# Kernel tuning notes

Hardware: AMD Instinct MI355X
Metric: run time of the kernel (lower is better)

## Reference

```python
import jax, jax.numpy as jnp
import numpy as np

N, H, MSG, OUT = 512, 128, 128, 64
F1, F2 = 256, 256  # f_dims (also used for g_mlp per source)
GOUT = 128         # hardcoded output_gmlp_dim
O1 = 256           # o_dims


def _p(key, shape, scale):
    return jax.random.normal(key, shape, dtype=jnp.float32) * scale


def setup_inputs() -> dict:
    key = jax.random.key(0)
    ks = jax.random.split(key, 24)
    s = lambda fan_in: 1.0 / np.sqrt(fan_in)
    inp = {
        "x": jax.random.normal(ks[0], (N, H), dtype=jnp.float32),
        "hidden": jax.random.normal(ks[1], (N, H), dtype=jnp.float32),
        "h0": jnp.zeros((1, N, H), dtype=jnp.float32),
        "c0": jnp.zeros((1, N, H), dtype=jnp.float32),
        # f MLP: 2H -> F1 -> F2 -> MSG
        "Wf1": _p(ks[2], (F1, 2 * H), s(2 * H)), "bf1": jnp.zeros((F1,), jnp.float32),
        "Wf2": _p(ks[3], (F2, F1), s(F1)), "bf2": jnp.zeros((F2,), jnp.float32),
        "Wf3": _p(ks[4], (MSG, F2), s(F2)), "bf3": jnp.zeros((MSG,), jnp.float32),
        # g_mlp: H+MSG -> F1 -> F2 -> GOUT
        "Wg1": _p(ks[5], (F1, H + MSG), s(H + MSG)), "bg1": jnp.zeros((F1,), jnp.float32),
        "Wg2": _p(ks[6], (F2, F1), s(F1)), "bg2": jnp.zeros((F2,), jnp.float32),
        "Wg3": _p(ks[7], (GOUT, F2), s(F2)), "bg3": jnp.zeros((GOUT,), jnp.float32),
        # LSTM (1 layer): GOUT -> H, gate order i,f,g,o
        "W_ih": _p(ks[8], (4 * H, GOUT), s(H)), "W_hh": _p(ks[9], (4 * H, H), s(H)),
        "b_ih": jnp.zeros((4 * H,), jnp.float32), "b_hh": jnp.zeros((4 * H,), jnp.float32),
        # o MLP: H -> O1 -> OUT
        "Wo1": _p(ks[10], (O1, H), s(H)), "bo1": jnp.zeros((O1,), jnp.float32),
        "Wo2": _p(ks[11], (OUT, O1), s(O1)), "bo2": jnp.zeros((OUT,), jnp.float32),
    }
    return inp


def reference(x, hidden, h0, c0,
              Wf1, bf1, Wf2, bf2, Wf3, bf3,
              Wg1, bg1, Wg2, bg2, Wg3, bg3,
              W_ih, W_hh, b_ih, b_hh,
              Wo1, bo1, Wo2, bo2):
    # --- pairwise message MLP f(cat(hidden[i], hidden[j])) over all (i,j) ---
    # split first-layer weight to avoid materializing [N,N,2H] concat
    A = hidden @ Wf1[:, :H].T            # [N, F1], contribution of node i
    B = hidden @ Wf1[:, H:].T            # [N, F1], contribution of node j
    h1 = jax.nn.relu(A[:, None, :] + B[None, :, :] + bf1)   # [N, N, F1]
    h2 = jax.nn.relu(h1 @ Wf2.T + bf2)                       # [N, N, F2]
    messages = h2 @ Wf3.T + bf3                              # [N, N, MSG]
    sum_messages = jnp.sum(messages, axis=0)                 # [N, MSG] (sum over i)

    # --- g_mlp on cat(x, sum_messages) ---
    g_in = jnp.concatenate([x, sum_messages], axis=1)        # [N, H+MSG]
    g1 = jax.nn.relu(g_in @ Wg1.T + bg1)
    g2 = jax.nn.relu(g1 @ Wg2.T + bg2)
    input_g = g2 @ Wg3.T + bg3                               # [N, GOUT]

    # --- single-step LSTM (seq_len=1, batch=N), PyTorch gate order i,f,g,o ---
    gates = input_g @ W_ih.T + b_ih + h0[0] @ W_hh.T + b_hh  # [N, 4H]
    i_g, f_g, g_g, o_g = jnp.split(gates, 4, axis=1)
    i_g = jax.nn.sigmoid(i_g); f_g = jax.nn.sigmoid(f_g)
    g_g = jnp.tanh(g_g); o_g = jax.nn.sigmoid(o_g)
    c_new = f_g * c0[0] + i_g * g_g
    hidden_new = o_g * jnp.tanh(c_new)                       # [N, H]

    # --- output MLP o (single_output=False) ---
    o1 = jax.nn.relu(hidden_new @ Wo1.T + bo1)
    out = o1 @ Wo2.T + bo2                                   # [N, OUT]

    return (out, hidden_new, hidden_new[None], c_new[None])
```

## Files before the change

kernel.cpp:

```cpp
#include <hip/hip_runtime.h>
#include <hip/hip_bf16.h>


#define NN   512
#define HH   128
#define F1D  256
#define F2D  256
#define OUTD 64
#define ICHUNK 64

typedef _Float16 half_t;
typedef _Float16 half4 __attribute__((ext_vector_type(4)));
typedef _Float16 half8 __attribute__((ext_vector_type(8)));
typedef float float4_t __attribute__((ext_vector_type(4)));
typedef float float8_t __attribute__((ext_vector_type(8)));

__device__ __forceinline__ float sigmoidf_(float x) {
    return 1.0f / (1.0f + __expf(-x));
}

#define HL_INV 2.44140625e-4f

#define WS_TAIL_B 1835008
#define T3H 0
#define G1H 65536
#define G2H 196608
#define G3H 327680
#define CATH 393216
#define O1H 655360
#define O2H 720896

__constant__ int c_cumblk[7] = {32, 96, 160, 192, 320, 352, 368};
__constant__ int c_hioff[7]  = {T3H, G1H, G2H, G3H, CATH, O1H, O2H};
__constant__ int c_cnt[7]    = {32768, 65536, 65536, 32768, 131072, 32768, 16384};
__constant__ int c_K[7]      = {256, 256, 256, 256, 256, 128, 256};

__global__ __launch_bounds__(256)
void k0_prep(const float* __restrict__ Wf3,
             const float* __restrict__ Wg1, const float* __restrict__ Wg2,
             const float* __restrict__ Wg3,
             const float* __restrict__ W_ih, const float* __restrict__ W_hh,
             const float* __restrict__ Wo1, const float* __restrict__ Wo2,
             half_t* __restrict__ tail) {
    const int t = threadIdx.x;
    const int bid = blockIdx.x;
    int m = 0;
    while (m < 6 && bid >= c_cumblk[m]) ++m;
    const int startblk = (m == 0) ? 0 : c_cumblk[m - 1];
    const int e0 = (bid - startblk) * 1024 + t * 4;
    const int K = c_K[m];

    float4_t v;
    if (m == 4) {
        const int n = e0 >> 8, k = e0 & 255;
        v = (k < 128) ? *(const float4_t*)(W_ih + n * 128 + k)
                      : *(const float4_t*)(W_hh + n * 128 + (k - 128));
    } else {
        const float* src;
        switch (m) {
            case 0: src = Wf3; break;
            case 1: src = Wg1; break;
            case 2: src = Wg2; break;
            case 3: src = Wg3; break;
            case 5: src = Wo1; break;
            default: src = Wo2; break;
        }
        v = *(const float4_t*)(src + e0);
    }
    const int n = e0 / K, k = e0 % K;
    const int panel = n >> 4, l15 = n & 15;
    const int ks = k >> 5, g4 = (k >> 3) & 3, e = k & 7;
    const int fidx = panel * (K << 4) + ks * 512 + ((g4 << 4) + l15) * 8 + e;

    half4 hv, lv;
#pragma unroll
    for (int q = 0; q < 4; ++q) {
        half_t h = (half_t)v[q];
        hv[q] = h;
        lv[q] = (half_t)((v[q] - (float)h) * 4096.0f);
    }
    *(half4*)(tail + c_hioff[m] + fidx) = hv;
    *(half4*)(tail + c_hioff[m] + c_cnt[m] + fidx) = lv;
}

__global__ void k1_proj(const float* __restrict__ hidden,
                        const float* __restrict__ Wf1,
                        const float* __restrict__ bf1,
                        const float* __restrict__ Wf2,
                        float* __restrict__ A32,
                        float* __restrict__ B32,
                        half_t* __restrict__ Whi,
                        half_t* __restrict__ Wlo) {
    __shared__ float hid[4][HH];
    const int t = threadIdx.x;
    const int i0 = blockIdx.x * 4;
    for (int q = t; q < 4 * HH; q += 256)
        hid[q >> 7][q & 127] = hidden[(i0 + (q >> 7)) * HH + (q & 127)];
    __syncthreads();

    float accA[4], accB[4];
    const float b = bf1[t];
#pragma unroll
    for (int r = 0; r < 4; ++r) { accA[r] = b; accB[r] = 0.0f; }

    const float* wr = Wf1 + t * 256;
#pragma unroll 4
    for (int k = 0; k < HH; k += 4) {
        float4_t wa = *(const float4_t*)(wr + k);
        float4_t wb = *(const float4_t*)(wr + HH + k);
#pragma unroll
        for (int r = 0; r < 4; ++r) {
            const float* hp = &hid[r][k];
            accA[r] += wa[0]*hp[0] + wa[1]*hp[1] + wa[2]*hp[2] + wa[3]*hp[3];
            accB[r] += wb[0]*hp[0] + wb[1]*hp[1] + wb[2]*hp[2] + wb[3]*hp[3];
        }
    }
#pragma unroll
    for (int r = 0; r < 4; ++r) {
        A32[(i0 + r) * F1D + t] = accA[r];
        B32[(i0 + r) * F1D + t] = accB[r];
    }
    for (int q = t; q < 512; q += 256) {
        int idx = blockIdx.x * 512 + q;
        float wv = Wf2[idx];
        half_t hi = (half_t)wv;
        Whi[idx] = hi;
        Wlo[idx] = (half_t)((wv - (float)hi) * 4096.0f);
    }
}

__global__ __launch_bounds__(512, 2)
void k2_pairwise(const float* __restrict__ A32,
                 const float* __restrict__ B32,
                 const half_t* __restrict__ Whi,
                 const half_t* __restrict__ Wlo,
                 const float* __restrict__ bf2,
                 float* __restrict__ S) {
    __shared__ half_t hbuf[2][8][512];

    const int tid = threadIdx.x;
    const int lane = tid & 63;
    const int w = tid >> 6;
    const int l15 = lane & 15;
    const int g4 = lane >> 4;
    const int j0 = blockIdx.y * 16;
    const int i0 = blockIdx.x * ICHUNK;

    half8 Wh[2][8], Wl[2][8];
#pragma unroll
    for (int nt = 0; nt < 2; ++nt)
#pragma unroll
        for (int ks = 0; ks < 8; ++ks) {
            const size_t off = (size_t)(w*32 + nt*16 + l15) * F1D + ks*32 + g4*8;
            Wh[nt][ks] = *(const half8*)(Whi + off);
            Wl[nt][ks] = *(const half8*)(Wlo + off);
        }

    const float8_t Bw = *(const float8_t*)(B32 + (size_t)(j0 + l15) * F1D + w*32 + g4*8);

    float b2v[2];
#pragma unroll
    for (int nt = 0; nt < 2; ++nt) b2v[nt] = bf2[w*32 + nt*16 + l15];

    float4_t acc[2];
#pragma unroll
    for (int nt = 0; nt < 2; ++nt)
#pragma unroll
        for (int r = 0; r < 4; ++r) acc[nt][r] = 0.0f;

    {
        float8_t a = *(const float8_t*)(A32 + (size_t)i0 * F1D + w*32 + g4*8);
        float8_t s = a + Bw;
        half8 hf;
#pragma unroll
        for (int e = 0; e < 8; ++e) hf[e] = (half_t)fmaxf(s[e], 0.0f);
        *(half8*)&hbuf[0][w][lane * 8] = hf;
    }
    __syncthreads();

    int p = 0;
    for (int io = 0; io < ICHUNK; ++io) {
        float8_t a;
        if (io + 1 < ICHUNK)
            a = *(const float8_t*)(A32 + (size_t)(i0 + io + 1) * F1D + w*32 + g4*8);

        float4_t C[2], Cl[2];
#pragma unroll
        for (int nt = 0; nt < 2; ++nt)
#pragma unroll
            for (int r = 0; r < 4; ++r) { C[nt][r] = 0.0f; Cl[nt][r] = 0.0f; }

#pragma unroll
        for (int ks = 0; ks < 8; ++ks) {
            half8 hf = *(const half8*)&hbuf[p][ks][lane * 8];
            C[0]  = __builtin_amdgcn_mfma_f32_16x16x32_f16(hf, Wh[0][ks], C[0], 0, 0, 0);
            C[1]  = __builtin_amdgcn_mfma_f32_16x16x32_f16(hf, Wh[1][ks], C[1], 0, 0, 0);
            Cl[0] = __builtin_amdgcn_mfma_f32_16x16x32_f16(hf, Wl[0][ks], Cl[0], 0, 0, 0);
            Cl[1] = __builtin_amdgcn_mfma_f32_16x16x32_f16(hf, Wl[1][ks], Cl[1], 0, 0, 0);
        }

        if (io + 1 < ICHUNK) {
            float8_t s = a + Bw;
            half8 hf;
#pragma unroll
            for (int e = 0; e < 8; ++e) hf[e] = (half_t)fmaxf(s[e], 0.0f);
            *(half8*)&hbuf[p ^ 1][w][lane * 8] = hf;
        }

#pragma unroll
        for (int nt = 0; nt < 2; ++nt) {
#pragma unroll
            for (int r = 0; r < 4; ++r) {
                float v = fmaf(Cl[nt][r], HL_INV, C[nt][r]) + b2v[nt];
                acc[nt][r] += fmaxf(v, 0.0f);
            }
        }
        __syncthreads();
        p ^= 1;
    }

#pragma unroll
    for (int nt = 0; nt < 2; ++nt)
#pragma unroll
        for (int r = 0; r < 4; ++r)
            atomicAdd(&S[(size_t)(j0 + g4*4 + r) * F2D + w*32 + nt*16 + l15], acc[nt][r]);
}

#define AST 260

template<int NT, int NKS>
__device__ __forceinline__ void frag_gemm(const float* __restrict__ aPtr,
                                          const half_t* __restrict__ WhF,
                                          const half_t* __restrict__ WlF,
                                          const int* pB, int lane8,
                                          float4_t* Chi, float4_t* Clo) {
#pragma unroll
    for (int ks = 0; ks < NKS; ++ks) {
        float4_t a0 = *(const float4_t*)(aPtr + ks * 32);
        float4_t a1 = *(const float4_t*)(aPtr + ks * 32 + 4);
        half8 ah, al;
#pragma unroll
        for (int e = 0; e < 4; ++e) {
            half_t h0 = (half_t)a0[e];
            ah[e] = h0; al[e] = (half_t)((a0[e] - (float)h0) * 4096.0f);
            half_t h1 = (half_t)a1[e];
            ah[4+e] = h1; al[4+e] = (half_t)((a1[e] - (float)h1) * 4096.0f);
        }
#pragma unroll
        for (int nt = 0; nt < NT; ++nt) {
            half8 wh = *(const half8*)(WhF + pB[nt] + ks * 512 + lane8);
            half8 wl = *(const half8*)(WlF + pB[nt] + ks * 512 + lane8);
            Chi[nt] = __builtin_amdgcn_mfma_f32_16x16x32_f16(ah, wh, Chi[nt], 0, 0, 0);
            Clo[nt] = __builtin_amdgcn_mfma_f32_16x16x32_f16(ah, wl, Clo[nt], 0, 0, 0);
            Clo[nt] = __builtin_amdgcn_mfma_f32_16x16x32_f16(al, wh, Clo[nt], 0, 0, 0);
        }
    }
}

__global__ __launch_bounds__(512)
void k4_tail(const float* __restrict__ S,
             const float* __restrict__ x,
             const float* __restrict__ h0,
             const float* __restrict__ c0,
             const half_t* __restrict__ tail,
             const float* __restrict__ bf3,
             const float* __restrict__ bg1, const float* __restrict__ bg2,
             const float* __restrict__ bg3,
             const float* __restrict__ b_ih, const float* __restrict__ b_hh,
             const float* __restrict__ bo1, const float* __restrict__ bo2,
             float* __restrict__ out,
             float* __restrict__ hid_out,
             float* __restrict__ h_out,
             float* __restrict__ c_out) {
    __shared__ float bufA[16 * AST];
    __shared__ float bufB[16 * AST];
    __shared__ float bufC[16 * AST];
    const int tid = threadIdx.x;
    const int lane = tid & 63;
    const int w = tid >> 6;
    const int l15 = lane & 15;
    const int g4 = lane >> 4;
    const int r0 = blockIdx.x * 16;
    const int lane8 = lane * 8;

    for (int q = tid; q < 16 * 256; q += 512)
        bufC[(q >> 8) * AST + (q & 255)] = S[(size_t)(r0 + (q >> 8)) * 256 + (q & 255)];
    for (int q = tid; q < 16 * 128; q += 512)
        bufA[(q >> 7) * AST + (q & 127)] = x[(r0 + (q >> 7)) * 128 + (q & 127)];
    __syncthreads();

    const float* aFrag;
    int pB[4];
    float4_t Chi[4], Clo[4];

    {
        const int n = w * 16 + l15;
        pB[0] = w * 4096;
        Chi[0] = float4_t{0,0,0,0}; Clo[0] = float4_t{0,0,0,0};
        aFrag = bufC + l15 * AST + g4 * 8;
        frag_gemm<1, 8>(aFrag, tail + T3H, tail + T3H + 32768, pB, lane8, Chi, Clo);
        const float b = 512.0f * bf3[n];
#pragma unroll
        for (int r = 0; r < 4; ++r)
            bufA[(g4 * 4 + r) * AST + 128 + n] = Chi[0][r] + Clo[0][r] * HL_INV + b;
    }
    __syncthreads();

    {
        pB[0] = (w * 2) * 4096; pB[1] = (w * 2 + 1) * 4096;
        Chi[0] = float4_t{0,0,0,0}; Clo[0] = float4_t{0,0,0,0};
        Chi[1] = float4_t{0,0,0,0}; Clo[1] = float4_t{0,0,0,0};
        aFrag = bufA + l15 * AST + g4 * 8;
        frag_gemm<2, 8>(aFrag, tail + G1H, tail + G1H + 65536, pB, lane8, Chi, Clo);
#pragma unroll
        for (int nt = 0; nt < 2; ++nt) {
            const int n = w * 32 + nt * 16 + l15;
            const float b = bg1[n];
#pragma unroll
            for (int r = 0; r < 4; ++r)
                bufB[(g4 * 4 + r) * AST + n] = fmaxf(Chi[nt][r] + Clo[nt][r] * HL_INV + b, 0.0f);
        }
    }
    __syncthreads();

    {
        pB[0] = (w * 2) * 4096; pB[1] = (w * 2 + 1) * 4096;
        Chi[0] = float4_t{0,0,0,0}; Clo[0] = float4_t{0,0,0,0};
        Chi[1] = float4_t{0,0,0,0}; Clo[1] = float4_t{0,0,0,0};
        aFrag = bufB + l15 * AST + g4 * 8;
        frag_gemm<2, 8>(aFrag, tail + G2H, tail + G2H + 65536, pB, lane8, Chi, Clo);
#pragma unroll
        for (int nt = 0; nt < 2; ++nt) {
            const int n = w * 32 + nt * 16 + l15;
            const float b = bg2[n];
#pragma unroll
            for (int r = 0; r < 4; ++r)
                bufC[(g4 * 4 + r) * AST + n] = fmaxf(Chi[nt][r] + Clo[nt][r] * HL_INV + b, 0.0f);
        }
        for (int q = tid; q < 16 * 128; q += 512)
            bufA[(q >> 7) * AST + 128 + (q & 127)] = h0[(r0 + (q >> 7)) * 128 + (q & 127)];
    }
    __syncthreads();

    {
        const int n = w * 16 + l15;
        pB[0] = w * 4096;
        Chi[0] = float4_t{0,0,0,0}; Clo[0] = float4_t{0,0,0,0};
        aFrag = bufC + l15 * AST + g4 * 8;
        frag_gemm<1, 8>(aFrag, tail + G3H, tail + G3H + 32768, pB, lane8, Chi, Clo);
        const float b = bg3[n];
#pragma unroll
        for (int r = 0; r < 4; ++r)
            bufA[(g4 * 4 + r) * AST + n] = Chi[0][r] + Clo[0][r] * HL_INV + b;
    }
    __syncthreads();

    {
#pragma unroll
        for (int nt = 0; nt < 4; ++nt) {
            pB[nt] = (w + nt * 8) * 4096;
            Chi[nt] = float4_t{0,0,0,0}; Clo[nt] = float4_t{0,0,0,0};
        }
        aFrag = bufA + l15 * AST + g4 * 8;
        frag_gemm<4, 8>(aFrag, tail + CATH, tail + CATH + 131072, pB, lane8, Chi, Clo);

        const int nh = w * 16 + l15;
        float bi = b_ih[nh]       + b_hh[nh];
        float bf = b_ih[128 + nh] + b_hh[128 + nh];
        float bg = b_ih[256 + nh] + b_hh[256 + nh];
        float bo = b_ih[384 + nh] + b_hh[384 + nh];
#pragma unroll
        for (int r = 0; r < 4; ++r) {
            const int row = r0 + g4 * 4 + r;
            float gi = sigmoidf_(Chi[0][r] + Clo[0][r] * HL_INV + bi);
            float gf = sigmoidf_(Chi[1][r] + Clo[1][r] * HL_INV + bf);
            float gg = tanhf(    Chi[2][r] + Clo[2][r] * HL_INV + bg);
            float go = sigmoidf_(Chi[3][r] + Clo[3][r] * HL_INV + bo);
            float c = gf * c0[row * 128 + nh] + gi * gg;
            float h = go * tanhf(c);
            bufC[(g4 * 4 + r) * AST + nh] = h;
            hid_out[row * 128 + nh] = h;
            h_out[row * 128 + nh]   = h;
            c_out[row * 128 + nh]   = c;
        }
    }
    __syncthreads();

    {
        pB[0] = (w * 2) * 2048; pB[1] = (w * 2 + 1) * 2048;
        Chi[0] = float4_t{0,0,0,0}; Clo[0] = float4_t{0,0,0,0};
        Chi[1] = float4_t{0,0,0,0}; Clo[1] = float4_t{0,0,0,0};
        aFrag = bufC + l15 * AST + g4 * 8;
        frag_gemm<2, 4>(aFrag, tail + O1H, tail + O1H + 32768, pB, lane8, Chi, Clo);
#pragma unroll
        for (int nt = 0; nt < 2; ++nt) {
            const int n = w * 32 + nt * 16 + l15;
            const float b = bo1[n];
#pragma unroll
            for (int r = 0; r < 4; ++r)
                bufB[(g4 * 4 + r) * AST + n] = fmaxf(Chi[nt][r] + Clo[nt][r] * HL_INV + b, 0.0f);
        }
    }
    __syncthreads();

    if (w < 4) {
        const int n = w * 16 + l15;
        pB[0] = w * 4096;
        Chi[0] = float4_t{0,0,0,0}; Clo[0] = float4_t{0,0,0,0};
        aFrag = bufB + l15 * AST + g4 * 8;
        frag_gemm<1, 8>(aFrag, tail + O2H, tail + O2H + 16384, pB, lane8, Chi, Clo);
        const float b = bo2[n];
#pragma unroll
        for (int r = 0; r < 4; ++r)
            out[(r0 + g4 * 4 + r) * OUTD + n] = Chi[0][r] + Clo[0][r] * HL_INV + b;
    }
}

extern "C" void kernel_launch(void* const* d_in, const int* in_sizes, int n_in,
                              void* d_out, int out_size, void* d_ws, size_t ws_size,
                              hipStream_t stream) {
    const float* x      = (const float*)d_in[0];
    const float* hidden = (const float*)d_in[1];
    const float* h0     = (const float*)d_in[2];
    const float* c0     = (const float*)d_in[3];
    const float* Wf1    = (const float*)d_in[4];
    const float* bf1    = (const float*)d_in[5];
    const float* Wf2    = (const float*)d_in[6];
    const float* bf2    = (const float*)d_in[7];
    const float* Wf3    = (const float*)d_in[8];
    const float* bf3    = (const float*)d_in[9];
    const float* Wg1    = (const float*)d_in[10];
    const float* bg1    = (const float*)d_in[11];
    const float* Wg2    = (const float*)d_in[12];
    const float* bg2    = (const float*)d_in[13];
    const float* Wg3    = (const float*)d_in[14];
    const float* bg3    = (const float*)d_in[15];
    const float* W_ih   = (const float*)d_in[16];
    const float* W_hh   = (const float*)d_in[17];
    const float* b_ih   = (const float*)d_in[18];
    const float* b_hh   = (const float*)d_in[19];
    const float* Wo1    = (const float*)d_in[20];
    const float* bo1    = (const float*)d_in[21];
    const float* Wo2    = (const float*)d_in[22];
    const float* bo2    = (const float*)d_in[23];

    char* wsb = (char*)d_ws;
    float*  A32  = (float*)(wsb + 0);
    float*  B32  = (float*)(wsb + 524288);
    half_t* Whi  = (half_t*)(wsb + 1048576);
    half_t* Wlo  = (half_t*)(wsb + 1179648);
    float*  S    = (float*)(wsb + 1310720);
    half_t* tail = (half_t*)(wsb + WS_TAIL_B);

    float* outp  = (float*)d_out;
    float* hid1  = (float*)d_out + 32768;
    float* hid2  = (float*)d_out + 98304;
    float* cout  = (float*)d_out + 163840;

    hipMemsetAsync(S, 0, (size_t)NN * F2D * sizeof(float), stream);

    k0_prep<<<dim3(368), dim3(256), 0, stream>>>(Wf3, Wg1, Wg2, Wg3,
                                                 W_ih, W_hh, Wo1, Wo2, tail);

    k1_proj<<<dim3(128), dim3(256), 0, stream>>>(hidden, Wf1, bf1, Wf2,
                                                 A32, B32, Whi, Wlo);

    k2_pairwise<<<dim3(8, 32), dim3(512), 0, stream>>>(A32, B32, Whi, Wlo, bf2, S);

    k4_tail<<<dim3(32), dim3(512), 0, stream>>>(S, x, h0, c0, tail,
                                                bf3, bg1, bg2, bg3,
                                                b_ih, b_hh, bo1, bo2,
                                                outp, hid1, hid2, cout);
}
```

Measured before the change: 223.8 us.

## Pre-swizzle Wf2 into MFMA fragment layout and transpose Wf1 for coalesced projection

```diff
diff --git a/kernel.cpp b/kernel.cpp
--- a/kernel.cpp
+++ b/kernel.cpp
@@ -10,7 +10,6 @@
 #define ICHUNK 64
 
 typedef _Float16 half_t;
-typedef _Float16 half4 __attribute__((ext_vector_type(4)));
 typedef _Float16 half8 __attribute__((ext_vector_type(8)));
 typedef float float4_t __attribute__((ext_vector_type(4)));
 typedef float float8_t __attribute__((ext_vector_type(8)));
@@ -22,6 +21,7 @@
 #define HL_INV 2.44140625e-4f
 
 #define WS_TAIL_B 1835008
+#define WS_WT1_B  3342336
 #define T3H 0
 #define G1H 65536
 #define G2H 196608
@@ -30,67 +30,105 @@
 #define O1H 655360
 #define O2H 720896
 
-__constant__ int c_cumblk[7] = {32, 96, 160, 192, 320, 352, 368};
-__constant__ int c_hioff[7]  = {T3H, G1H, G2H, G3H, CATH, O1H, O2H};
-__constant__ int c_cnt[7]    = {32768, 65536, 65536, 32768, 131072, 32768, 16384};
-__constant__ int c_K[7]      = {256, 256, 256, 256, 256, 128, 256};
+__constant__ int p_cum[8]   = {16, 24, 40, 56, 64, 96, 112, 116};
+__constant__ int p_K[8]     = {256, 256, 256, 256, 256, 256, 128, 256};
+__constant__ int p_hioff[8] = {0, T3H, G1H, G2H, G3H, CATH, O1H, O2H};
+__constant__ int p_cnt[8]   = {65536, 32768, 65536, 65536, 32768, 131072, 32768, 16384};
 
 __global__ __launch_bounds__(256)
-void k0_prep(const float* __restrict__ Wf3,
+void k0_prep(const float* __restrict__ Wf1,
+             const float* __restrict__ Wf2,
+             const float* __restrict__ Wf3,
              const float* __restrict__ Wg1, const float* __restrict__ Wg2,
              const float* __restrict__ Wg3,
              const float* __restrict__ W_ih, const float* __restrict__ W_hh,
              const float* __restrict__ Wo1, const float* __restrict__ Wo2,
-             half_t* __restrict__ tail) {
+             half_t* __restrict__ tail,
+             half_t* __restrict__ W2H, half_t* __restrict__ W2L,
+             float* __restrict__ WT1) {
+    __shared__ float slab[4096];
+    __shared__ float tile[64][65];
     const int t = threadIdx.x;
     const int bid = blockIdx.x;
-    int m = 0;
-    while (m < 6 && bid >= c_cumblk[m]) ++m;
-    const int startblk = (m == 0) ? 0 : c_cumblk[m - 1];
-    const int e0 = (bid - startblk) * 1024 + t * 4;
-    const int K = c_K[m];
-
-    float4_t v;
-    if (m == 4) {
-        const int n = e0 >> 8, k = e0 & 255;
-        v = (k < 128) ? *(const float4_t*)(W_ih + n * 128 + k)
-                      : *(const float4_t*)(W_hh + n * 128 + (k - 128));
-    } else {
+
+    if (bid < 116) {
+        int m = 0;
+        while (m < 7 && bid >= p_cum[m]) ++m;
+        const int pl = bid - (m ? p_cum[m - 1] : 0);
+        const int K = p_K[m];
+        const int kshift = (K == 256) ? 8 : 7;
+        const int n0 = pl * 16;
+
         const float* src;
         switch (m) {
-            case 0: src = Wf3; break;
-            case 1: src = Wg1; break;
-            case 2: src = Wg2; break;
-            case 3: src = Wg3; break;
-            case 5: src = Wo1; break;
+            case 0: src = Wf2; break;
+            case 1: src = Wf3; break;
+            case 2: src = Wg1; break;
+            case 3: src = Wg2; break;
+            case 4: src = Wg3; break;
+            case 6: src = Wo1; break;
             default: src = Wo2; break;
         }
-        v = *(const float4_t*)(src + e0);
-    }
-    const int n = e0 / K, k = e0 % K;
-    const int panel = n >> 4, l15 = n & 15;
-    const int ks = k >> 5, g4 = (k >> 3) & 3, e = k & 7;
-    const int fidx = panel * (K << 4) + ks * 512 + ((g4 << 4) + l15) * 8 + e;
-
-    half4 hv, lv;
-#pragma unroll
-    for (int q = 0; q < 4; ++q) {
-        half_t h = (half_t)v[q];
-        hv[q] = h;
-        lv[q] = (half_t)((v[q] - (float)h) * 4096.0f);
-    }
-    *(half4*)(tail + c_hioff[m] + fidx) = hv;
-    *(half4*)(tail + c_hioff[m] + c_cnt[m] + fidx) = lv;
-}
-
-__global__ void k1_proj(const float* __restrict__ hidden,
-                        const float* __restrict__ Wf1,
-                        const float* __restrict__ bf1,
-                        const float* __restrict__ Wf2,
-                        float* __restrict__ A32,
-                        float* __restrict__ B32,
-                        half_t* __restrict__ Whi,
-                        half_t* __restrict__ Wlo) {
+        for (int q = t; q < (16 * K) / 4; q += 256) {
+            const int flat = q * 4;
+            const int r = flat >> kshift;
+            const int k = flat & (K - 1);
+            float4_t v;
+            if (m == 5) {
+                v = (k < 128) ? *(const float4_t*)(W_ih + (n0 + r) * 128 + k)
+                              : *(const float4_t*)(W_hh + (n0 + r) * 128 + (k - 128));
+            } else {
+                v = *(const float4_t*)(src + (size_t)(n0 + r) * K + k);
+            }
+            *(float4_t*)&slab[flat] = v;
+        }
+        __syncthreads();
+
+        half_t *hi, *lo;
+        if (m == 0) { hi = W2H; lo = W2L; }
+        else        { hi = tail + p_hioff[m]; lo = hi + p_cnt[m]; }
+        const int base = pl * (K << 4);
+        for (int f0 = t * 8; f0 < 16 * K; f0 += 2048) {
+            const int ks = f0 >> 9;
+            const int g4 = (f0 >> 7) & 3;
+            const int l15 = (f0 >> 3) & 15;
+            const int k0 = ks * 32 + g4 * 8;
+            float8_t v = *(const float8_t*)&slab[l15 * K + k0];
+            half8 hv, lv;
+#pragma unroll
+            for (int e = 0; e < 8; ++e) {
+                half_t h = (half_t)v[e];
+                hv[e] = h;
+                lv[e] = (half_t)((v[e] - (float)h) * 4096.0f);
+            }
+            *(half8*)(hi + base + f0) = hv;
+            *(half8*)(lo + base + f0) = lv;
+        }
+    } else {
+        const int local = bid - 116;
+        const int tr = local >> 2, tc = local & 3;
+#pragma unroll
+        for (int q = 0; q < 16; ++q) {
+            const int idx = q * 256 + t;
+            const int ly = idx >> 6, lx = idx & 63;
+            tile[ly][lx] = Wf1[(tr * 64 + ly) * 256 + tc * 64 + lx];
+        }
+        __syncthreads();
+#pragma unroll
+        for (int q = 0; q < 16; ++q) {
+            const int idx = q * 256 + t;
+            const int ly = idx >> 6, lx = idx & 63;
+            WT1[(tc * 64 + ly) * 256 + tr * 64 + lx] = tile[lx][ly];
+        }
+    }
+}
+
+__global__ __launch_bounds__(256)
+void k1_proj(const float* __restrict__ hidden,
+             const float* __restrict__ WT1,
+             const float* __restrict__ bf1,
+             float* __restrict__ A32,
+             float* __restrict__ B32) {
     __shared__ float hid[4][HH];
     const int t = threadIdx.x;
     const int i0 = blockIdx.x * 4;
@@ -103,16 +141,16 @@
 #pragma unroll
     for (int r = 0; r < 4; ++r) { accA[r] = b; accB[r] = 0.0f; }
 
-    const float* wr = Wf1 + t * 256;
+    const float* wcol = WT1 + t;
 #pragma unroll 4
-    for (int k = 0; k < HH; k += 4) {
-        float4_t wa = *(const float4_t*)(wr + k);
-        float4_t wb = *(const float4_t*)(wr + HH + k);
+    for (int kk = 0; kk < HH; ++kk) {
+        const float va = wcol[kk * 256];
+        const float vb = wcol[(kk + 128) * 256];
 #pragma unroll
         for (int r = 0; r < 4; ++r) {
-            const float* hp = &hid[r][k];
-            accA[r] += wa[0]*hp[0] + wa[1]*hp[1] + wa[2]*hp[2] + wa[3]*hp[3];
-            accB[r] += wb[0]*hp[0] + wb[1]*hp[1] + wb[2]*hp[2] + wb[3]*hp[3];
+            const float h = hid[r][kk];
+            accA[r] = fmaf(h, va, accA[r]);
+            accB[r] = fmaf(h, vb, accB[r]);
         }
     }
 #pragma unroll
@@ -120,20 +158,13 @@
         A32[(i0 + r) * F1D + t] = accA[r];
         B32[(i0 + r) * F1D + t] = accB[r];
     }
-    for (int q = t; q < 512; q += 256) {
-        int idx = blockIdx.x * 512 + q;
-        float wv = Wf2[idx];
-        half_t hi = (half_t)wv;
-        Whi[idx] = hi;
-        Wlo[idx] = (half_t)((wv - (float)hi) * 4096.0f);
-    }
 }
 
 __global__ __launch_bounds__(512, 2)
 void k2_pairwise(const float* __restrict__ A32,
                  const float* __restrict__ B32,
-                 const half_t* __restrict__ Whi,
-                 const half_t* __restrict__ Wlo,
+                 const half_t* __restrict__ W2H,
+                 const half_t* __restrict__ W2L,
                  const float* __restrict__ bf2,
                  float* __restrict__ S) {
     __shared__ half_t hbuf[2][8][512];
@@ -146,21 +177,33 @@
     const int j0 = blockIdx.y * 16;
     const int i0 = blockIdx.x * ICHUNK;
 
+    const half8* WH8 = (const half8*)W2H;
+    const half8* WL8 = (const half8*)W2L;
     half8 Wh[2][8], Wl[2][8];
 #pragma unroll
     for (int nt = 0; nt < 2; ++nt)
 #pragma unroll
         for (int ks = 0; ks < 8; ++ks) {
-            const size_t off = (size_t)(w*32 + nt*16 + l15) * F1D + ks*32 + g4*8;
-            Wh[nt][ks] = *(const half8*)(Whi + off);
-            Wl[nt][ks] = *(const half8*)(Wlo + off);
-        }
-
-    const float8_t Bw = *(const float8_t*)(B32 + (size_t)(j0 + l15) * F1D + w*32 + g4*8);
+            const int idx = (w * 2 + nt) * 512 + ks * 64 + lane;
+            Wh[nt][ks] = WH8[idx];
+            Wl[nt][ks] = WL8[idx];
+        }
+#pragma unroll
+    for (int nt = 0; nt < 2; ++nt)
+#pragma unroll
+        for (int ks = 0; ks < 8; ++ks) {
+            asm volatile("" : "+v"(Wh[nt][ks]));
+            asm volatile("" : "+v"(Wl[nt][ks]));
+        }
+
+    float4_t Bw0 = *(const float4_t*)(B32 + (size_t)(j0 + l15) * F1D + w * 32 + g4 * 8);
+    float4_t Bw1 = *(const float4_t*)(B32 + (size_t)(j0 + l15) * F1D + w * 32 + g4 * 8 + 4);
+    asm volatile("" : "+v"(Bw0));
+    asm volatile("" : "+v"(Bw1));
 
     float b2v[2];
 #pragma unroll
-    for (int nt = 0; nt < 2; ++nt) b2v[nt] = bf2[w*32 + nt*16 + l15];
+    for (int nt = 0; nt < 2; ++nt) b2v[nt] = bf2[w * 32 + nt * 16 + l15];
 
     float4_t acc[2];
 #pragma unroll
@@ -169,20 +212,27 @@
         for (int r = 0; r < 4; ++r) acc[nt][r] = 0.0f;
 
     {
-        float8_t a = *(const float8_t*)(A32 + (size_t)i0 * F1D + w*32 + g4*8);
-        float8_t s = a + Bw;
+        const float* Ap = A32 + (size_t)i0 * F1D + w * 32 + g4 * 8;
+        float4_t a0 = *(const float4_t*)Ap;
+        float4_t a1 = *(const float4_t*)(Ap + 4);
         half8 hf;
 #pragma unroll
-        for (int e = 0; e < 8; ++e) hf[e] = (half_t)fmaxf(s[e], 0.0f);
+        for (int e = 0; e < 4; ++e) {
+            hf[e]     = (half_t)fmaxf(a0[e] + Bw0[e], 0.0f);
+            hf[4 + e] = (half_t)fmaxf(a1[e] + Bw1[e], 0.0f);
+        }
         *(half8*)&hbuf[0][w][lane * 8] = hf;
     }
     __syncthreads();
 
     int p = 0;
     for (int io = 0; io < ICHUNK; ++io) {
-        float8_t a;
-        if (io + 1 < ICHUNK)
-            a = *(const float8_t*)(A32 + (size_t)(i0 + io + 1) * F1D + w*32 + g4*8);
+        float4_t a0, a1;
+        if (io + 1 < ICHUNK) {
+            const float* Ap = A32 + (size_t)(i0 + io + 1) * F1D + w * 32 + g4 * 8;
+            a0 = *(const float4_t*)Ap;
+            a1 = *(const float4_t*)(Ap + 4);
+        }
 
         float4_t C[2], Cl[2];
 #pragma unroll
@@ -200,10 +250,12 @@
         }
 
         if (io + 1 < ICHUNK) {
-            float8_t s = a + Bw;
             half8 hf;
 #pragma unroll
-            for (int e = 0; e < 8; ++e) hf[e] = (half_t)fmaxf(s[e], 0.0f);
+            for (int e = 0; e < 4; ++e) {
+                hf[e]     = (half_t)fmaxf(a0[e] + Bw0[e], 0.0f);
+                hf[4 + e] = (half_t)fmaxf(a1[e] + Bw1[e], 0.0f);
+            }
             *(half8*)&hbuf[p ^ 1][w][lane * 8] = hf;
         }
 
@@ -223,7 +275,7 @@
     for (int nt = 0; nt < 2; ++nt)
 #pragma unroll
         for (int r = 0; r < 4; ++r)
-            atomicAdd(&S[(size_t)(j0 + g4*4 + r) * F2D + w*32 + nt*16 + l15], acc[nt][r]);
+            atomicAdd(&S[(size_t)(j0 + g4 * 4 + r) * F2D + w * 32 + nt * 16 + l15], acc[nt][r]);
 }
 
 #define AST 260
@@ -447,10 +499,11 @@
     char* wsb = (char*)d_ws;
     float*  A32  = (float*)(wsb + 0);
     float*  B32  = (float*)(wsb + 524288);
-    half_t* Whi  = (half_t*)(wsb + 1048576);
-    half_t* Wlo  = (half_t*)(wsb + 1179648);
+    half_t* W2H  = (half_t*)(wsb + 1048576);
+    half_t* W2L  = (half_t*)(wsb + 1179648);
     float*  S    = (float*)(wsb + 1310720);
     half_t* tail = (half_t*)(wsb + WS_TAIL_B);
+    float*  WT1  = (float*)(wsb + WS_WT1_B);
 
     float* outp  = (float*)d_out;
     float* hid1  = (float*)d_out + 32768;
@@ -459,13 +512,13 @@
 
     hipMemsetAsync(S, 0, (size_t)NN * F2D * sizeof(float), stream);
 
-    k0_prep<<<dim3(368), dim3(256), 0, stream>>>(Wf3, Wg1, Wg2, Wg3,
-                                                 W_ih, W_hh, Wo1, Wo2, tail);
-
-    k1_proj<<<dim3(128), dim3(256), 0, stream>>>(hidden, Wf1, bf1, Wf2,
-                                                 A32, B32, Whi, Wlo);
-
-    k2_pairwise<<<dim3(8, 32), dim3(512), 0, stream>>>(A32, B32, Whi, Wlo, bf2, S);
+    k0_prep<<<dim3(132), dim3(256), 0, stream>>>(Wf1, Wf2, Wf3, Wg1, Wg2, Wg3,
+                                                 W_ih, W_hh, Wo1, Wo2,
+                                                 tail, W2H, W2L, WT1);
+
+    k1_proj<<<dim3(128), dim3(256), 0, stream>>>(hidden, WT1, bf1, A32, B32);
+
+    k2_pairwise<<<dim3(8, 32), dim3(512), 0, stream>>>(A32, B32, W2H, W2L, bf2, S);
 
     k4_tail<<<dim3(32), dim3(512), 0, stream>>>(S, x, h0, c0, tail,
                                                 bf3, bg1, bg2, bg3,
```

Measured after the change: 213.6 us. 1.05x faster.
